# Kernel tuning notes

Measured on AMD Instinct MI355X. Metric: run time of the kernel, lower is better.

## Reference

```python
import jax, jax.numpy as jnp
import numpy as np

N_NODES = 100000
N_EDGES = 1600000
D_FEAT = 512
HEADS = 8
UNITS1 = 8          # layer1: 8 heads x 8 units, concat -> 64
HIDDEN = HEADS * UNITS1
OUT_DIM = 16        # layer2: 8 heads x 16 units, avg -> 16
N_IDX = 10000
NEG_SLOPE = 0.2     # LeakyReLU slope used by GAT attention


def _gat_layer(x, edges, W, a_src, a_dst, merge):
    """One multi-head GAT layer.
    x: [N, F], edges: [E, 2] with (dst, src) columns,
    W: [F, H, U], a_src/a_dst: [H, U].
    """
    n = x.shape[0]
    dst = edges[:, 0]
    src = edges[:, 1]
    h = jnp.einsum('nf,fhu->nhu', x, W)                      # [N, H, U]
    # per-node attention score halves, then gather per edge (cheaper than
    # gathering full features first)
    s_src = jnp.einsum('nhu,hu->nh', h, a_src)               # [N, H]
    s_dst = jnp.einsum('nhu,hu->nh', h, a_dst)               # [N, H]
    e = s_dst[dst] + s_src[src]                              # [E, H]
    e = jnp.where(e > 0, e, NEG_SLOPE * e)                   # LeakyReLU
    # segment softmax over incoming edges of each dst node (stable)
    m = jax.ops.segment_max(e, dst, num_segments=n)          # [N, H]
    m = jnp.where(jnp.isfinite(m), m, 0.0)                   # empty segments
    ex = jnp.exp(e - m[dst])                                 # [E, H]
    denom = jax.ops.segment_sum(ex, dst, num_segments=n)     # [N, H]
    alpha = ex / jnp.maximum(denom[dst], 1e-9)               # [E, H]
    msg = h[src] * alpha[:, :, None]                         # [E, H, U]
    out = jax.ops.segment_sum(msg, dst, num_segments=n)      # [N, H, U]
    if merge == 'concat':
        return out.reshape(n, -1)                            # [N, H*U]
    return out.mean(axis=1)                                  # [N, U]


def setup_inputs() -> dict:
    key = jax.random.key(0)
    ks = jax.random.split(key, 9)
    node_states = jax.random.normal(ks[0], (N_NODES, D_FEAT), dtype=jnp.float32)
    edges = jax.random.randint(ks[1], (N_EDGES, 2), 0, N_NODES, dtype=jnp.int32).astype(jnp.int64)
    indices = jax.random.randint(ks[2], (N_IDX,), 0, N_NODES, dtype=jnp.int32).astype(jnp.int64)
    W1 = jax.random.normal(ks[3], (D_FEAT, HEADS, UNITS1), dtype=jnp.float32) / np.sqrt(D_FEAT)
    a1_src = jax.random.normal(ks[4], (HEADS, UNITS1), dtype=jnp.float32) / np.sqrt(UNITS1)
    a1_dst = jax.random.normal(ks[5], (HEADS, UNITS1), dtype=jnp.float32) / np.sqrt(UNITS1)
    W2 = jax.random.normal(ks[6], (HIDDEN, HEADS, OUT_DIM), dtype=jnp.float32) / np.sqrt(HIDDEN)
    a2_src = jax.random.normal(ks[7], (HEADS, OUT_DIM), dtype=jnp.float32) / np.sqrt(OUT_DIM)
    a2_dst = jax.random.normal(ks[8], (HEADS, OUT_DIM), dtype=jnp.float32) / np.sqrt(OUT_DIM)
    return {
        'node_states': node_states, 'edges': edges, 'indices': indices,
        'W1': W1, 'a1_src': a1_src, 'a1_dst': a1_dst,
        'W2': W2, 'a2_src': a2_src, 'a2_dst': a2_dst,
    }


def reference(node_states, edges, indices, W1, a1_src, a1_dst, W2, a2_src, a2_dst):
    # layer 1: concat merge + ELU nonlinearity (standard GAT hidden layer)
    x = _gat_layer(node_states, edges, W1, a1_src, a1_dst, merge='concat')
    x = jax.nn.elu(x)                                        # [N, 64]
    # layer 2: average merge, linear output logits
    out = _gat_layer(x, edges, W2, a2_src, a2_dst, merge='avg')  # [N, OUT_DIM]
    return jnp.take(out, indices, axis=0)                    # [N_IDX, OUT_DIM]
```

## Files before the change

kernel.cpp:

```cpp
#include <hip/hip_runtime.h>
#include <hip/hip_bf16.h>

#define NN 100000
#define NE 1600000
#define DF 512
#define NIDX 10000

#define NBKT 512
#define BKT_W 196
#define EDGES_PER_BKT_BLK 3125
#define GEMM1_NB 782
#define GEMM1A 391
#define GEMM1B (GEMM1_NB - GEMM1A)

typedef __attribute__((ext_vector_type(8))) short short8v;
typedef __attribute__((ext_vector_type(4))) float float4v;

__device__ __forceinline__ float eluf(float x) { return x > 0.f ? x : expm1f(x); }
__device__ __forceinline__ float lrelu(float x) { return x > 0.f ? x : 0.2f * x; }
__device__ __forceinline__ ushort f2bf(float f) {
  __hip_bfloat16 b = __float2bfloat16(f);
  return *(ushort*)&b;
}

__device__ __forceinline__ void glds16(const void* gsrc, void* ldst) {
  __builtin_amdgcn_global_load_lds(
      (const __attribute__((address_space(1))) uint32_t*)(uintptr_t)gsrc,
      (__attribute__((address_space(3))) uint32_t*)(uintptr_t)ldst, 16, 0, 0);
}

__global__ __launch_bounds__(256) void prep_w_hist(const float* __restrict__ W1,
                                                   ushort* __restrict__ Wt_hi, ushort* __restrict__ Wt_lo,
                                                   const int2* __restrict__ edges, int* __restrict__ bkt_cnt) {
  const int tid = threadIdx.x;
  if (blockIdx.x >= 128) {
    __shared__ int h[NBKT];
    h[tid] = 0; h[tid + 256] = 0;
    __syncthreads();
    const int b = blockIdx.x - 128;
    const int i0 = b * EDGES_PER_BKT_BLK;
    const int i1 = min(i0 + EDGES_PER_BKT_BLK, NE);
    for (int i = i0 + tid; i < i1; i += 256) atomicAdd(&h[edges[i].x / BKT_W], 1);
    __syncthreads();
    if (h[tid]) atomicAdd(&bkt_cnt[tid], h[tid]);
    if (h[tid + 256]) atomicAdd(&bkt_cnt[tid + 256], h[tid + 256]);
    return;
  }
  int t = blockIdx.x * 256 + tid;
  int k = t >> 6, n = t & 63;
  float w = W1[t];
  ushort hi = f2bf(w);
  __hip_bfloat16 hb = *(__hip_bfloat16*)&hi;
  ushort lo = f2bf(w - __bfloat162float(hb));
  Wt_hi[(size_t)n * DF + k] = hi;
  Wt_lo[(size_t)n * DF + k] = lo;
}

#define BSTRIDE 40
template<int TAIL>
__global__ __launch_bounds__(256) void gemm1_mix(const float* __restrict__ x,
                                                 const ushort* __restrict__ Wt_hi, const ushort* __restrict__ Wt_lo,
                                                 const float* __restrict__ a1s, const float* __restrict__ a1d,
                                                 ushort* __restrict__ h1b, float* __restrict__ s_src,
                                                 float* __restrict__ s_dst,
                                                 int gemm_cnt, int gemm_off,
                                                 const int2* __restrict__ edges, int* __restrict__ bkt_cursor,
                                                 uint* __restrict__ pairs,
                                                 const int* __restrict__ bkt_base, int* __restrict__ row_off,
                                                 int* __restrict__ ssrc) {
  __shared__ __align__(16) char smem[53248];
  const int tid = threadIdx.x;

  if (blockIdx.x >= (unsigned)gemm_cnt) {
    const int tb = blockIdx.x - gemm_cnt;
    if (TAIL == 0) {
      int* h = (int*)smem;
      int* lbase = h + NBKT;
      int* cur = lbase + NBKT;
      h[tid] = 0; h[tid + 256] = 0;
      __syncthreads();
      const int i0 = tb * EDGES_PER_BKT_BLK;
      const int i1 = min(i0 + EDGES_PER_BKT_BLK, NE);
      for (int i = i0 + tid; i < i1; i += 256) atomicAdd(&h[edges[i].x / BKT_W], 1);
      __syncthreads();
#pragma unroll
      for (int q = 0; q < 2; ++q) {
        int b = tid + q * 256;
        int c = h[b];
        lbase[b] = c ? atomicAdd(&bkt_cursor[b], c) : 0;
        cur[b] = 0;
      }
      __syncthreads();
      for (int i = i0 + tid; i < i1; i += 256) {
        int2 e = edges[i];
        int bk = e.x / BKT_W;
        int r = atomicAdd(&cur[bk], 1);
        pairs[lbase[bk] + r] = ((uint)(e.x - bk * BKT_W) << 24) | (uint)e.y;
      }
    } else {
      int* hist = (int*)smem;
      int* ts = hist + 256;
      int* cur = ts + 256;
      const int d0 = tb * BKT_W;
      if (d0 >= NN) return;
      const int nd = min(BKT_W, NN - d0);
      const int beg = bkt_base[tb], end = bkt_base[tb + 1];
      hist[tid] = 0;
      __syncthreads();
      for (int i = beg + tid; i < end; i += 256) atomicAdd(&hist[pairs[i] >> 24], 1);
      __syncthreads();
      int v = hist[tid];
      ts[tid] = v;
      __syncthreads();
      for (int off = 1; off < 256; off <<= 1) {
        int t2 = (tid >= off) ? ts[tid - off] : 0;
        __syncthreads();
        ts[tid] += t2;
        __syncthreads();
      }
      int excl = ts[tid] - v;
      if (tid < nd) row_off[d0 + tid] = beg + excl;
      cur[tid] = beg + excl;
      __syncthreads();
      for (int i = beg + tid; i < end; i += 256) {
        uint p = pairs[i];
        int pos = atomicAdd(&cur[p >> 24], 1);
        ssrc[pos] = (int)(p & 0xFFFFFFu);
      }
    }
    return;
  }

  float* Abuf[2];
  Abuf[0] = (float*)smem;
  Abuf[1] = (float*)(smem + 16384);
  ushort* Bhi[2]; ushort* Blo[2];
  Bhi[0] = (ushort*)(smem + 32768);
  Blo[0] = Bhi[0] + 64 * BSTRIDE;
  Bhi[1] = Blo[0] + 64 * BSTRIDE;
  Blo[1] = Bhi[1] + 64 * BSTRIDE;
  float* Cs = (float*)smem;

  const int mb = (gemm_off + blockIdx.x) * 128;
  const int wave = tid >> 6, l = tid & 63;
  const int wm = wave * 32;
  const int lm = l & 15, kq = l >> 4, kg = kq * 8;

  float4v acc[2][4];
#pragma unroll
  for (int i = 0; i < 2; ++i)
#pragma unroll
    for (int j = 0; j < 4; ++j) acc[i][j] = (float4v){0.f, 0.f, 0.f, 0.f};

  size_t asrc[4];
#pragma unroll
  for (int i = 0; i < 4; ++i) {
    int g = mb + wm + 8 * i + (l >> 3);
    if (g > NN - 1) g = NN - 1;
    asrc[i] = (size_t)g * DF + (l & 7) * 4;
  }
  const int bn = tid & 63, bk = (tid >> 6) * 8;

  {
    uint4 rbh = *(const uint4*)&Wt_hi[(size_t)bn * DF + bk];
    uint4 rbl = *(const uint4*)&Wt_lo[(size_t)bn * DF + bk];
    asm volatile("" ::: "memory");
#pragma unroll
    for (int i = 0; i < 4; ++i)
      glds16(x + asrc[i], (char*)Abuf[0] + wave * 4096 + i * 1024);
    *(uint4*)&Bhi[0][bn * BSTRIDE + bk] = rbh;
    *(uint4*)&Blo[0][bn * BSTRIDE + bk] = rbl;
    asm volatile("s_waitcnt lgkmcnt(0)" ::: "memory");
    __builtin_amdgcn_s_barrier();
  }

  for (int ks = 0; ks < 16; ++ks) {
    const int k0 = ks * 32;
    const int cur = ks & 1;
    uint4 rbh, rbl;
    if (ks < 15) {
      rbh = *(const uint4*)&Wt_hi[(size_t)bn * DF + k0 + 32 + bk];
      rbl = *(const uint4*)&Wt_lo[(size_t)bn * DF + k0 + 32 + bk];
      asm volatile("" ::: "memory");
#pragma unroll
      for (int i = 0; i < 4; ++i)
        glds16(x + asrc[i] + k0 + 32, (char*)Abuf[cur ^ 1] + wave * 4096 + i * 1024);
      asm volatile("s_waitcnt vmcnt(6)" ::: "memory");
    } else {
      asm volatile("s_waitcnt vmcnt(0)" ::: "memory");
    }
    short8v ah[2], al[2];
#pragma unroll
    for (int mt = 0; mt < 2; ++mt) {
      const float* p = Abuf[cur] + wave * 1024 + (mt * 16 + lm) * 32 + kg;
      float4 f0 = *(const float4*)p;
      float4 f1 = *(const float4*)(p + 4);
      float f[8] = {f0.x, f0.y, f0.z, f0.w, f1.x, f1.y, f1.z, f1.w};
#pragma unroll
      for (int c = 0; c < 8; ++c) {
        uint u = __float_as_uint(f[c]);
        ah[mt][c] = (short)(u >> 16);
        float hf = __uint_as_float(u & 0xFFFF0000u);
        al[mt][c] = (short)(__float_as_uint(f[c] - hf) >> 16);
      }
    }
    short8v bh[4], bl[4];
#pragma unroll
    for (int nt = 0; nt < 4; ++nt) {
      bh[nt] = *(const short8v*)&Bhi[cur][(nt * 16 + lm) * BSTRIDE + kg];
      bl[nt] = *(const short8v*)&Blo[cur][(nt * 16 + lm) * BSTRIDE + kg];
    }
#pragma unroll
    for (int mt = 0; mt < 2; ++mt)
#pragma unroll
      for (int nt = 0; nt < 4; ++nt) {
        acc[mt][nt] = __builtin_amdgcn_mfma_f32_16x16x32_bf16(ah[mt], bh[nt], acc[mt][nt], 0, 0, 0);
        acc[mt][nt] = __builtin_amdgcn_mfma_f32_16x16x32_bf16(ah[mt], bl[nt], acc[mt][nt], 0, 0, 0);
        acc[mt][nt] = __builtin_amdgcn_mfma_f32_16x16x32_bf16(al[mt], bh[nt], acc[mt][nt], 0, 0, 0);
      }
    if (ks < 15) {
      *(uint4*)&Bhi[cur ^ 1][bn * BSTRIDE + bk] = rbh;
      *(uint4*)&Blo[cur ^ 1][bn * BSTRIDE + bk] = rbl;
      asm volatile("s_waitcnt lgkmcnt(0)" ::: "memory");
    }
    __builtin_amdgcn_s_barrier();
  }

  __syncthreads();

#pragma unroll
  for (int mt = 0; mt < 2; ++mt)
#pragma unroll
    for (int nt = 0; nt < 4; ++nt)
#pragma unroll
      for (int r = 0; r < 4; ++r)
        Cs[(wm + mt * 16 + kq * 4 + r) * 65 + nt * 16 + lm] = acc[mt][nt][r];
  __syncthreads();

  {
    int row = tid >> 1, c0 = (tid & 1) * 32;
    int g = mb + row;
    if (g < NN) {
      uint u[16];
#pragma unroll
      for (int j = 0; j < 16; ++j) {
        uint p0 = f2bf(Cs[row * 65 + c0 + 2 * j]);
        uint p1 = f2bf(Cs[row * 65 + c0 + 2 * j + 1]);
        u[j] = p0 | (p1 << 16);
      }
#pragma unroll
      for (int q = 0; q < 4; ++q)
        *(uint4*)&h1b[(size_t)g * 64 + c0 + 8 * q] = *(uint4*)&u[4 * q];
      int half = tid & 1;
      float4 ssv, ddv;
      float* ssp = &ssv.x;
      float* ddp = &ddv.x;
#pragma unroll
      for (int hq = 0; hq < 4; ++hq) {
        int hh = half * 4 + hq;
        float ss = 0.f, dd = 0.f;
#pragma unroll
        for (int u8 = 0; u8 < 8; ++u8) {
          float hv = Cs[row * 65 + hh * 8 + u8];
          ss = fmaf(hv, a1s[hh * 8 + u8], ss);
          dd = fmaf(hv, a1d[hh * 8 + u8], dd);
        }
        ssp[hq] = ss; ddp[hq] = dd;
      }
      *(float4*)&s_src[(size_t)g * 8 + half * 4] = ssv;
      *(float4*)&s_dst[(size_t)g * 8 + half * 4] = ddv;
    }
  }
}

__global__ __launch_bounds__(NBKT) void bkt_scan_kernel(const int* __restrict__ bkt_cnt, int* __restrict__ bkt_base,
                                                        int* __restrict__ bkt_cursor, int* __restrict__ row_off) {
  __shared__ int s[NBKT];
  int tid = threadIdx.x;
  int v = bkt_cnt[tid];
  s[tid] = v;
  __syncthreads();
  for (int off = 1; off < NBKT; off <<= 1) {
    int t = (tid >= off) ? s[tid - off] : 0;
    __syncthreads();
    s[tid] += t;
    __syncthreads();
  }
  int excl = s[tid] - v;
  bkt_base[tid] = excl;
  bkt_cursor[tid] = excl;
  if (tid == NBKT - 1) bkt_base[NBKT] = s[tid];
  if (tid == 0) row_off[NN] = NE;
}

__global__ __launch_bounds__(256) void gemm2_fused(const float* __restrict__ A, const float* __restrict__ B,
                                                   __hip_bfloat162* __restrict__ Cb,
                                                   const float* __restrict__ a2s, const float* __restrict__ a2d,
                                                   float* __restrict__ s_src, float* __restrict__ s_dst,
                                                   int M) {
  __shared__ float sm[6528];
  float* As = sm;
  float* Bs = sm + 32 * 68;
  const int tid = threadIdx.x;
  const int m0 = blockIdx.x * 64;
  const int tx = tid & 15, ty = tid >> 4;
  float acc[4][8] = {};
  for (int k0 = 0; k0 < 64; k0 += 32) {
    for (int j = tid; j < 512; j += 256) {
      int r = j >> 3, kq = j & 7;
      int row = m0 + r;
      float4 v = make_float4(0.f, 0.f, 0.f, 0.f);
      if (row < M) v = *(const float4*)&A[(size_t)row * 64 + k0 + kq * 4];
      v.x = eluf(v.x); v.y = eluf(v.y); v.z = eluf(v.z); v.w = eluf(v.w);
      As[(kq * 4 + 0) * 68 + r] = v.x; As[(kq * 4 + 1) * 68 + r] = v.y;
      As[(kq * 4 + 2) * 68 + r] = v.z; As[(kq * 4 + 3) * 68 + r] = v.w;
    }
    for (int j = tid; j < 1024; j += 256) {
      int kr = j >> 5, nq = j & 31;
      *(float4*)&Bs[kr * 136 + nq * 4] = *(const float4*)&B[(size_t)(k0 + kr) * 128 + nq * 4];
    }
    __syncthreads();
#pragma unroll
    for (int kk = 0; kk < 32; ++kk) {
      float4 a4 = *(const float4*)&As[kk * 68 + ty * 4];
      float4 b0 = *(const float4*)&Bs[kk * 136 + tx * 8];
      float4 b1 = *(const float4*)&Bs[kk * 136 + tx * 8 + 4];
      float av[4] = {a4.x, a4.y, a4.z, a4.w};
      float bv[8] = {b0.x, b0.y, b0.z, b0.w, b1.x, b1.y, b1.z, b1.w};
#pragma unroll
      for (int i = 0; i < 4; ++i)
#pragma unroll
        for (int jj = 0; jj < 8; ++jj)
          acc[i][jj] = fmaf(av[i], bv[jj], acc[i][jj]);
    }
    __syncthreads();
  }
  const int hx = tx >> 1, half8 = (tx & 1) * 8;
#pragma unroll
  for (int i = 0; i < 4; ++i) {
    int row = m0 + ty * 4 + i;
    float ss = 0.f, dd = 0.f;
#pragma unroll
    for (int c = 0; c < 8; ++c) {
      ss = fmaf(acc[i][c], a2s[hx * 16 + half8 + c], ss);
      dd = fmaf(acc[i][c], a2d[hx * 16 + half8 + c], dd);
    }
    ss += __shfl_xor(ss, 1, 64);
    dd += __shfl_xor(dd, 1, 64);
    if (row < M) {
      uint u[4];
#pragma unroll
      for (int q = 0; q < 4; ++q)
        u[q] = (uint)f2bf(acc[i][2 * q]) | ((uint)f2bf(acc[i][2 * q + 1]) << 16);
      *(uint4*)&Cb[(size_t)row * 64 + tx * 4] = *(uint4*)u;
      if ((tx & 1) == 0) {
        s_src[(size_t)row * 8 + hx] = ss;
        s_dst[(size_t)row * 8 + hx] = dd;
      }
    }
  }
}

__global__ __launch_bounds__(256) void agg1_kernel(const int* __restrict__ row_off, const int* __restrict__ srcs,
                                                   const float* __restrict__ s_src, const float* __restrict__ s_dst,
                                                   const __hip_bfloat16* __restrict__ hb, float* __restrict__ out, int n) {
  int wave = (blockIdx.x * 256 + threadIdx.x) >> 6;
  int lane = threadIdx.x & 63;
  if (wave >= n) return;
  int hh = lane >> 3;
  float sd = s_dst[(size_t)wave * 8 + hh];
  int beg = row_off[wave], end = row_off[wave + 1];
  float acc = 0.f, den = 0.f;
  int i = beg;
  for (; i + 8 <= end; i += 8) {
    int s[8];
#pragma unroll
    for (int j = 0; j < 8; ++j) s[j] = srcs[i + j];
    float e[8], hv[8];
#pragma unroll
    for (int j = 0; j < 8; ++j) e[j] = s_src[(size_t)s[j] * 8 + hh];
#pragma unroll
    for (int j = 0; j < 8; ++j) hv[j] = __bfloat162float(hb[(size_t)s[j] * 64 + lane]);
#pragma unroll
    for (int j = 0; j < 8; ++j) {
      float xj = __expf(lrelu(sd + e[j]));
      den += xj;
      acc = fmaf(xj, hv[j], acc);
    }
  }
  for (; i < end; ++i) {
    int s0 = srcs[i];
    float x0 = __expf(lrelu(sd + s_src[(size_t)s0 * 8 + hh]));
    den += x0;
    acc = fmaf(x0, __bfloat162float(hb[(size_t)s0 * 64 + lane]), acc);
  }
  out[(size_t)wave * 64 + lane] = acc / fmaxf(den, 1e-9f);
}

__global__ __launch_bounds__(256) void agg2_idx_kernel(const int* __restrict__ row_off, const int* __restrict__ srcs,
                                                       const float* __restrict__ s_src, const float* __restrict__ s_dst,
                                                       const __hip_bfloat162* __restrict__ h2b, const int* __restrict__ idx,
                                                       float* __restrict__ out, int ni) {
  int w = (blockIdx.x * 256 + threadIdx.x) >> 6;
  int lane = threadIdx.x & 63;
  if (w >= ni) return;
  int node = idx[w];
  int hh = lane >> 3, o2 = lane & 7;
  float sd = s_dst[(size_t)node * 8 + hh];
  int beg = row_off[node], end = row_off[node + 1];
  float a0 = 0.f, a1 = 0.f, den = 0.f;
  int i = beg;
  for (; i + 4 <= end; i += 4) {
    int s0 = srcs[i], s1 = srcs[i + 1], s2 = srcs[i + 2], s3 = srcs[i + 3];
    float e0 = s_src[(size_t)s0 * 8 + hh];
    float e1 = s_src[(size_t)s1 * 8 + hh];
    float e2 = s_src[(size_t)s2 * 8 + hh];
    float e3 = s_src[(size_t)s3 * 8 + hh];
    float2 v0 = __bfloat1622float2(h2b[(size_t)s0 * 64 + hh * 8 + o2]);
    float2 v1 = __bfloat1622float2(h2b[(size_t)s1 * 64 + hh * 8 + o2]);
    float2 v2 = __bfloat1622float2(h2b[(size_t)s2 * 64 + hh * 8 + o2]);
    float2 v3 = __bfloat1622float2(h2b[(size_t)s3 * 64 + hh * 8 + o2]);
    float x0 = __expf(lrelu(sd + e0));
    float x1 = __expf(lrelu(sd + e1));
    float x2 = __expf(lrelu(sd + e2));
    float x3 = __expf(lrelu(sd + e3));
    den += (x0 + x1) + (x2 + x3);
    a0 = fmaf(x0, v0.x, fmaf(x1, v1.x, fmaf(x2, v2.x, fmaf(x3, v3.x, a0))));
    a1 = fmaf(x0, v0.y, fmaf(x1, v1.y, fmaf(x2, v2.y, fmaf(x3, v3.y, a1))));
  }
  for (; i < end; ++i) {
    int s0 = srcs[i];
    float x0 = __expf(lrelu(sd + s_src[(size_t)s0 * 8 + hh]));
    float2 v0 = __bfloat1622float2(h2b[(size_t)s0 * 64 + hh * 8 + o2]);
    den += x0;
    a0 = fmaf(x0, v0.x, a0);
    a1 = fmaf(x0, v0.y, a1);
  }
  float r0 = a0 / fmaxf(den, 1e-9f);
  float r1 = a1 / fmaxf(den, 1e-9f);
  for (int m = 8; m < 64; m <<= 1) {
    r0 += __shfl_xor(r0, m, 64);
    r1 += __shfl_xor(r1, m, 64);
  }
  if (lane < 8) {
    float2 wv = make_float2(r0 * 0.125f, r1 * 0.125f);
    *(float2*)&out[(size_t)w * 16 + lane * 2] = wv;
  }
}

extern "C" void kernel_launch(void* const* d_in, const int* in_sizes, int n_in,
                              void* d_out, int out_size, void* d_ws, size_t ws_size,
                              hipStream_t stream) {
  const float* x   = (const float*)d_in[0];
  const int2* edges = (const int2*)d_in[1];
  const int* indices = (const int*)d_in[2];
  const float* W1  = (const float*)d_in[3];
  const float* a1s = (const float*)d_in[4];
  const float* a1d = (const float*)d_in[5];
  const float* W2  = (const float*)d_in[6];
  const float* a2s = (const float*)d_in[7];
  const float* a2d = (const float*)d_in[8];
  float* out = (float*)d_out;

  char* ws = (char*)d_ws;
  size_t off = 0;
  auto alloc = [&](size_t bytes) {
    void* p = ws + off;
    off = (off + bytes + 255) & ~(size_t)255;
    return p;
  };
  float* s1src = (float*)alloc((size_t)NN * 8 * 4);
  float* s1dst = (float*)alloc((size_t)NN * 8 * 4);
  float* out1  = (float*)alloc((size_t)NN * 64 * 4);
  ushort* h1b  = (ushort*)alloc((size_t)NN * 64 * 2);
  __hip_bfloat162* h2b = (__hip_bfloat162*)alloc((size_t)NN * 128 * 2);
  int* row_off = (int*)alloc(((size_t)NN + 1) * 4);
  int* ssrc    = (int*)alloc((size_t)NE * 4);
  uint* pairs  = (uint*)alloc((size_t)NE * 4);
  ushort* Wt_hi = (ushort*)alloc((size_t)DF * 64 * 2);
  ushort* Wt_lo = (ushort*)alloc((size_t)DF * 64 * 2);
  int* bkt_cnt    = (int*)alloc(NBKT * 4);
  int* bkt_base   = (int*)alloc((NBKT + 1) * 4);
  int* bkt_cursor = (int*)alloc(NBKT * 4);

  hipMemsetAsync(bkt_cnt, 0, NBKT * 4, stream);

  dim3 b256(256);
  prep_w_hist<<<dim3(128 + NBKT), b256, 0, stream>>>(W1, Wt_hi, Wt_lo, edges, bkt_cnt);
  bkt_scan_kernel<<<dim3(1), dim3(NBKT), 0, stream>>>(bkt_cnt, bkt_base, bkt_cursor, row_off);
  gemm1_mix<0><<<dim3(GEMM1A + NBKT), b256, 0, stream>>>(x, Wt_hi, Wt_lo, a1s, a1d, h1b, s1src, s1dst,
                                                         GEMM1A, 0, edges, bkt_cursor, pairs,
                                                         bkt_base, row_off, ssrc);
  gemm1_mix<1><<<dim3(GEMM1B + NBKT), b256, 0, stream>>>(x, Wt_hi, Wt_lo, a1s, a1d, h1b, s1src, s1dst,
                                                         GEMM1B, GEMM1A, edges, bkt_cursor, pairs,
                                                         bkt_base, row_off, ssrc);
  agg1_kernel<<<dim3(NN / 4), b256, 0, stream>>>(row_off, ssrc, s1src, s1dst, (const __hip_bfloat16*)h1b, out1, NN);
  gemm2_fused<<<dim3((NN + 63) / 64), b256, 0, stream>>>(out1, W2, h2b, a2s, a2d, s1src, s1dst, NN);
  agg2_idx_kernel<<<dim3((NIDX * 64 + 255) / 256), b256, 0, stream>>>(row_off, ssrc, s1src, s1dst, h2b, indices, out, NIDX);
}
```

Measured before the change: 245.9 us.

## Fuse layer-1 aggregation into layer-2 GEMM via shared-memory tile

Merges the per-node layer-1 attention aggregation kernel into the layer-2 GEMM kernel. Each block aggregates 64 nodes (16 per wave), applies ELU, and writes the results straight into the shared A tile. This removes the fp32 out1 intermediate round trip through global memory and one kernel launch. In exchange the block count for the aggregation drops from 25000 to about 1563, with each wave processing 16 nodes in series, which may reduce latency hiding for the gather-heavy loop. Separate s2src/s2dst buffers replace the earlier overwrite of the layer-1 score arrays.

```diff
diff --git a/kernel.cpp b/kernel.cpp
--- a/kernel.cpp
+++ b/kernel.cpp
@@ -293,28 +293,60 @@
   if (tid == 0) row_off[NN] = NE;
 }
 
-__global__ __launch_bounds__(256) void gemm2_fused(const float* __restrict__ A, const float* __restrict__ B,
-                                                   __hip_bfloat162* __restrict__ Cb,
-                                                   const float* __restrict__ a2s, const float* __restrict__ a2d,
-                                                   float* __restrict__ s_src, float* __restrict__ s_dst,
-                                                   int M) {
-  __shared__ float sm[6528];
-  float* As = sm;
-  float* Bs = sm + 32 * 68;
+__global__ __launch_bounds__(256) void agg1_gemm2(const int* __restrict__ row_off, const int* __restrict__ srcs,
+                                                  const float* __restrict__ s_src, const float* __restrict__ s_dst,
+                                                  const __hip_bfloat16* __restrict__ hb,
+                                                  const float* __restrict__ B,
+                                                  __hip_bfloat162* __restrict__ Cb,
+                                                  const float* __restrict__ a2s, const float* __restrict__ a2d,
+                                                  float* __restrict__ s2src, float* __restrict__ s2dst) {
+  __shared__ float As[64 * 68];
+  __shared__ float Bs[32 * 136];
   const int tid = threadIdx.x;
-  const int m0 = blockIdx.x * 64;
+  const int nb = blockIdx.x * 64;
+  const int wave = tid >> 6, lane = tid & 63;
+  const int hh = lane >> 3;
+
+  for (int t = 0; t < 16; ++t) {
+    int local_m = wave * 16 + t;
+    int node = nb + local_m;
+    float r = 0.f;
+    if (node < NN) {
+      float sd = s_dst[(size_t)node * 8 + hh];
+      int beg = row_off[node], end = row_off[node + 1];
+      float acc = 0.f, den = 0.f;
+      int i = beg;
+      for (; i + 8 <= end; i += 8) {
+        int s[8];
+#pragma unroll
+        for (int j = 0; j < 8; ++j) s[j] = srcs[i + j];
+        float e[8], hv[8];
+#pragma unroll
+        for (int j = 0; j < 8; ++j) e[j] = s_src[(size_t)s[j] * 8 + hh];
+#pragma unroll
+        for (int j = 0; j < 8; ++j) hv[j] = __bfloat162float(hb[(size_t)s[j] * 64 + lane]);
+#pragma unroll
+        for (int j = 0; j < 8; ++j) {
+          float xj = __expf(lrelu(sd + e[j]));
+          den += xj;
+          acc = fmaf(xj, hv[j], acc);
+        }
+      }
+      for (; i < end; ++i) {
+        int s0 = srcs[i];
+        float x0 = __expf(lrelu(sd + s_src[(size_t)s0 * 8 + hh]));
+        den += x0;
+        acc = fmaf(x0, __bfloat162float(hb[(size_t)s0 * 64 + lane]), acc);
+      }
+      r = eluf(acc / fmaxf(den, 1e-9f));
+    }
+    As[lane * 68 + local_m] = r;
+  }
+  __syncthreads();
+
   const int tx = tid & 15, ty = tid >> 4;
   float acc[4][8] = {};
   for (int k0 = 0; k0 < 64; k0 += 32) {
-    for (int j = tid; j < 512; j += 256) {
-      int r = j >> 3, kq = j & 7;
-      int row = m0 + r;
-      float4 v = make_float4(0.f, 0.f, 0.f, 0.f);
-      if (row < M) v = *(const float4*)&A[(size_t)row * 64 + k0 + kq * 4];
-      v.x = eluf(v.x); v.y = eluf(v.y); v.z = eluf(v.z); v.w = eluf(v.w);
-      As[(kq * 4 + 0) * 68 + r] = v.x; As[(kq * 4 + 1) * 68 + r] = v.y;
-      As[(kq * 4 + 2) * 68 + r] = v.z; As[(kq * 4 + 3) * 68 + r] = v.w;
-    }
     for (int j = tid; j < 1024; j += 256) {
       int kr = j >> 5, nq = j & 31;
       *(float4*)&Bs[kr * 136 + nq * 4] = *(const float4*)&B[(size_t)(k0 + kr) * 128 + nq * 4];
@@ -322,7 +354,7 @@
     __syncthreads();
 #pragma unroll
     for (int kk = 0; kk < 32; ++kk) {
-      float4 a4 = *(const float4*)&As[kk * 68 + ty * 4];
+      float4 a4 = *(const float4*)&As[(k0 + kk) * 68 + ty * 4];
       float4 b0 = *(const float4*)&Bs[kk * 136 + tx * 8];
       float4 b1 = *(const float4*)&Bs[kk * 136 + tx * 8 + 4];
       float av[4] = {a4.x, a4.y, a4.z, a4.w};
@@ -338,7 +370,7 @@
   const int hx = tx >> 1, half8 = (tx & 1) * 8;
 #pragma unroll
   for (int i = 0; i < 4; ++i) {
-    int row = m0 + ty * 4 + i;
+    int row = nb + ty * 4 + i;
     float ss = 0.f, dd = 0.f;
 #pragma unroll
     for (int c = 0; c < 8; ++c) {
@@ -347,54 +379,18 @@
     }
     ss += __shfl_xor(ss, 1, 64);
     dd += __shfl_xor(dd, 1, 64);
-    if (row < M) {
+    if (row < NN) {
       uint u[4];
 #pragma unroll
       for (int q = 0; q < 4; ++q)
         u[q] = (uint)f2bf(acc[i][2 * q]) | ((uint)f2bf(acc[i][2 * q + 1]) << 16);
       *(uint4*)&Cb[(size_t)row * 64 + tx * 4] = *(uint4*)u;
       if ((tx & 1) == 0) {
-        s_src[(size_t)row * 8 + hx] = ss;
-        s_dst[(size_t)row * 8 + hx] = dd;
-      }
-    }
-  }
-}
-
-__global__ __launch_bounds__(256) void agg1_kernel(const int* __restrict__ row_off, const int* __restrict__ srcs,
-                                                   const float* __restrict__ s_src, const float* __restrict__ s_dst,
-                                                   const __hip_bfloat16* __restrict__ hb, float* __restrict__ out, int n) {
-  int wave = (blockIdx.x * 256 + threadIdx.x) >> 6;
-  int lane = threadIdx.x & 63;
-  if (wave >= n) return;
-  int hh = lane >> 3;
-  float sd = s_dst[(size_t)wave * 8 + hh];
-  int beg = row_off[wave], end = row_off[wave + 1];
-  float acc = 0.f, den = 0.f;
-  int i = beg;
-  for (; i + 8 <= end; i += 8) {
-    int s[8];
-#pragma unroll
-    for (int j = 0; j < 8; ++j) s[j] = srcs[i + j];
-    float e[8], hv[8];
-#pragma unroll
-    for (int j = 0; j < 8; ++j) e[j] = s_src[(size_t)s[j] * 8 + hh];
-#pragma unroll
-    for (int j = 0; j < 8; ++j) hv[j] = __bfloat162float(hb[(size_t)s[j] * 64 + lane]);
-#pragma unroll
-    for (int j = 0; j < 8; ++j) {
-      float xj = __expf(lrelu(sd + e[j]));
-      den += xj;
-      acc = fmaf(xj, hv[j], acc);
-    }
-  }
-  for (; i < end; ++i) {
-    int s0 = srcs[i];
-    float x0 = __expf(lrelu(sd + s_src[(size_t)s0 * 8 + hh]));
-    den += x0;
-    acc = fmaf(x0, __bfloat162float(hb[(size_t)s0 * 64 + lane]), acc);
-  }
-  out[(size_t)wave * 64 + lane] = acc / fmaxf(den, 1e-9f);
+        s2src[(size_t)row * 8 + hx] = ss;
+        s2dst[(size_t)row * 8 + hx] = dd;
+      }
+    }
+  }
 }
 
 __global__ __launch_bounds__(256) void agg2_idx_kernel(const int* __restrict__ row_off, const int* __restrict__ srcs,
@@ -471,7 +467,8 @@
   };
   float* s1src = (float*)alloc((size_t)NN * 8 * 4);
   float* s1dst = (float*)alloc((size_t)NN * 8 * 4);
-  float* out1  = (float*)alloc((size_t)NN * 64 * 4);
+  float* s2src = (float*)alloc((size_t)NN * 8 * 4);
+  float* s2dst = (float*)alloc((size_t)NN * 8 * 4);
   ushort* h1b  = (ushort*)alloc((size_t)NN * 64 * 2);
   __hip_bfloat162* h2b = (__hip_bfloat162*)alloc((size_t)NN * 128 * 2);
   int* row_off = (int*)alloc(((size_t)NN + 1) * 4);
@@ -494,7 +491,8 @@
   gemm1_mix<1><<<dim3(GEMM1B + NBKT), b256, 0, stream>>>(x, Wt_hi, Wt_lo, a1s, a1d, h1b, s1src, s1dst,
                                                          GEMM1B, GEMM1A, edges, bkt_cursor, pairs,
                                                          bkt_base, row_off, ssrc);
-  agg1_kernel<<<dim3(NN / 4), b256, 0, stream>>>(row_off, ssrc, s1src, s1dst, (const __hip_bfloat16*)h1b, out1, NN);
-  gemm2_fused<<<dim3((NN + 63) / 64), b256, 0, stream>>>(out1, W2, h2b, a2s, a2d, s1src, s1dst, NN);
-  agg2_idx_kernel<<<dim3((NIDX * 64 + 255) / 256), b256, 0, stream>>>(row_off, ssrc, s1src, s1dst, h2b, indices, out, NIDX);
-}
+  agg1_gemm2<<<dim3((NN + 63) / 64), b256, 0, stream>>>(row_off, ssrc, s1src, s1dst,
+                                                        (const __hip_bfloat16*)h1b, W2, h2b, a2s, a2d,
+                                                        s2src, s2dst);
+  agg2_idx_kernel<<<dim3((NIDX * 64 + 255) / 256), b256, 0, stream>>>(row_off, ssrc, s2src, s2dst, h2b, indices, out, NIDX);
+}
```

After: 340.7 us. +38.6%, slower.
